# Kernel optimization log

Measured on AMD Instinct MI355X. Metric: run time of the kernel, lower is better.

Reference implementation:

```python
import jax, jax.numpy as jnp
import numpy as np

DIM = 768
NUM_HEADS = 12
HEAD_DIM = DIM // NUM_HEADS
SCALE = HEAD_DIM ** -0.5


def setup_inputs() -> dict:
    key = jax.random.key(0)
    ks = jax.random.split(key, 7)
    B, N = 4, 2048
    s = DIM ** -0.5
    return {
        "x": jax.random.normal(ks[0], (B, N, DIM), dtype=jnp.float32),
        "attn_bias": jax.random.normal(ks[1], (1, NUM_HEADS, N, N), dtype=jnp.float32),
        "Wq": jax.random.normal(ks[2], (DIM, DIM), dtype=jnp.float32) * s,
        "Wk": jax.random.normal(ks[3], (DIM, DIM), dtype=jnp.float32) * s,
        "Wv": jax.random.normal(ks[4], (DIM, DIM), dtype=jnp.float32) * s,
        "Wp": jax.random.normal(ks[5], (DIM, DIM), dtype=jnp.float32) * s,
        "bp": jax.random.normal(ks[6], (DIM,), dtype=jnp.float32) * 0.02,
    }


def reference(x, attn_bias, Wq, Wk, Wv, Wp, bp):
    B, N, C = x.shape
    # Linear layers use y = x @ W.T (torch convention); split heads: [B,H,N,D]
    def heads(y):
        return y.reshape(B, N, NUM_HEADS, HEAD_DIM).transpose(0, 2, 1, 3)
    q = heads(x @ Wq.T)
    k = heads(x @ Wk.T)
    v = heads(x @ Wv.T)
    attn = jnp.einsum("bhnd,bhmd->bhnm", q, k) * SCALE + attn_bias
    attn = jax.nn.softmax(attn, axis=-1)
    out = jnp.einsum("bhnm,bhmd->bhnd", attn, v)
    out = out.transpose(0, 2, 1, 3).reshape(B, N, C)
    return out @ Wp.T + bp
```

## Files before the change

kernel.cpp:

```cpp
#include <hip/hip_runtime.h>
#include <hip/hip_bf16.h>

#define NTOK 2048
#define NHEADS 12
#define HDIM 64
#define DIM 768
#define BATCH 4
#define SC2_    0.18033688011112042f
#define LOG2E_  1.4426950408889634f
#define SHIFT2_ 23.083120654223415f

typedef __attribute__((ext_vector_type(8))) short short8;
typedef __attribute__((ext_vector_type(4))) float f32x4;
typedef __attribute__((ext_vector_type(16))) float f32x16;

__device__ __forceinline__ short f2bf(float f) {
  union { float f; unsigned u; } v; v.f = f;
  unsigned r = v.u + 0x7fffu + ((v.u >> 16) & 1u);
  return (short)(r >> 16);
}

__device__ __forceinline__ f32x4 mfma_bf16(short8 a, short8 b, f32x4 c) {
  return __builtin_amdgcn_mfma_f32_16x16x32_bf16(a, b, c, 0, 0, 0);
}

__device__ __forceinline__ f32x16 mfma32(short8 a, short8 b, f32x16 c) {
  return __builtin_amdgcn_mfma_f32_32x32x16_bf16(a, b, c, 0, 0, 0);
}

__device__ __forceinline__ void gload_lds16(const void* g, void* l) {
  __builtin_amdgcn_global_load_lds((const __attribute__((address_space(1))) void*)g,
                                   (__attribute__((address_space(3))) void*)l, 16, 0, 0);
}

__device__ __forceinline__ float exp2_hw(float x) {
  float r; asm("v_exp_f32 %0, %1" : "=v"(r) : "v"(x)); return r;
}

__device__ __forceinline__ unsigned cvt_pk_bf16(float lo, float hi) {
  unsigned r; asm("v_cvt_pk_bf16_f32 %0, %1, %2" : "=v"(r) : "v"(lo), "v"(hi)); return r;
}

__global__ void cvt_x(const float* __restrict__ src, short* __restrict__ dst) {
  int i = blockIdx.x * 256 + threadIdx.x;
  float4 v = ((const float4*)src)[i];
  short4 o; o.x = f2bf(v.x); o.y = f2bf(v.y); o.z = f2bf(v.z); o.w = f2bf(v.w);
  ((short4*)dst)[i] = o;
}

__global__ void cvt_w(const float* __restrict__ w0, const float* __restrict__ w1,
                      const float* __restrict__ w2, const float* __restrict__ w3,
                      short* __restrict__ d0, short* __restrict__ d1,
                      short* __restrict__ d2, short* __restrict__ d3) {
  int i = blockIdx.x * 256 + threadIdx.x;
  const float* s = blockIdx.y == 0 ? w0 : blockIdx.y == 1 ? w1 : blockIdx.y == 2 ? w2 : w3;
  short* d = blockIdx.y == 0 ? d0 : blockIdx.y == 1 ? d1 : blockIdx.y == 2 ? d2 : d3;
  float4 v = ((const float4*)s)[i];
  short4 o; o.x = f2bf(v.x); o.y = f2bf(v.y); o.z = f2bf(v.z); o.w = f2bf(v.w);
  ((short4*)d)[i] = o;
}

__device__ __forceinline__ void gemm_mainloop(const short* __restrict__ A,
                                              const short* __restrict__ B,
                                              int mbase, int nbase,
                                              short* As, short* Bs,
                                              f32x4 (&acc)[4][4], int lane, int w) {
  int lr = lane & 15, lg = lane >> 4;
  int wr = w >> 1, wc = w & 1;
  for (int kb = 0; kb < DIM; kb += 64) {
    if (kb) __syncthreads();
#pragma unroll
    for (int c = 0; c < 4; ++c) {
      int row = w * 32 + c * 8 + (lane >> 3);
      int sch = (lane & 7) ^ (row & 7);
      gload_lds16(A + (size_t)(mbase + row) * DIM + kb + sch * 8, (char*)As + w * 4096 + c * 1024);
      gload_lds16(B + (size_t)(nbase + row) * DIM + kb + sch * 8, (char*)Bs + w * 4096 + c * 1024);
    }
    __syncthreads();
#pragma unroll
    for (int ks = 0; ks < 2; ++ks) {
      short8 af[4], bf[4];
#pragma unroll
      for (int i = 0; i < 4; ++i) {
        int row = wr * 64 + i * 16 + lr;
        int ch = (ks * 4 + lg) ^ (row & 7);
        af[i] = *(const short8*)(As + row * 64 + ch * 8);
      }
#pragma unroll
      for (int j = 0; j < 4; ++j) {
        int row = wc * 64 + j * 16 + lr;
        int ch = (ks * 4 + lg) ^ (row & 7);
        bf[j] = *(const short8*)(Bs + row * 64 + ch * 8);
      }
#pragma unroll
      for (int i = 0; i < 4; ++i)
#pragma unroll
        for (int j = 0; j < 4; ++j)
          acc[i][j] = mfma_bf16(af[i], bf[j], acc[i][j]);
    }
  }
}

__global__ __launch_bounds__(256, 2) void gemm_qkv(const short* __restrict__ xb,
    const short* __restrict__ wq, const short* __restrict__ wk, const short* __restrict__ wv,
    short* __restrict__ Qh, short* __restrict__ Kh, short* __restrict__ Vt) {
  __shared__ __align__(16) short As[128 * 64];
  __shared__ __align__(16) short Bs[128 * 64];
  int nt = blockIdx.x, mt = blockIdx.y, z = blockIdx.z;
  const short* B = z == 0 ? wq : (z == 1 ? wk : wv);
  int tid = threadIdx.x, lane = tid & 63, w = tid >> 6;
  f32x4 acc[4][4] = {};
  gemm_mainloop(xb, B, mt * 128, nt * 128, As, Bs, acc, lane, w);
  int lr = lane & 15, lg = lane >> 4, wr = w >> 1, wc = w & 1;
  if (z < 2) {
    short* dst = z == 0 ? Qh : Kh;
#pragma unroll
    for (int i = 0; i < 4; ++i)
#pragma unroll
      for (int j = 0; j < 4; ++j) {
        int m = mt * 128 + wr * 64 + i * 16 + lg * 4;
        int n = nt * 128 + wc * 64 + j * 16 + lr;
        int bb = m >> 11, nn = m & 2047, hh = n >> 6, d = n & 63;
        size_t base = (((size_t)bb * NHEADS + hh) * NTOK + nn) * HDIM + d;
#pragma unroll
        for (int r = 0; r < 4; ++r)
          dst[base + (size_t)r * HDIM] = f2bf(acc[i][j][r]);
      }
  } else {
#pragma unroll
    for (int i = 0; i < 4; ++i)
#pragma unroll
      for (int j = 0; j < 4; ++j) {
        int m = mt * 128 + wr * 64 + i * 16 + lg * 4;
        int n = nt * 128 + wc * 64 + j * 16 + lr;
        int bb = m >> 11, nn = m & 2047, hh = n >> 6, d = n & 63;
        short4 pk;
        pk.x = f2bf(acc[i][j][0]); pk.y = f2bf(acc[i][j][1]);
        pk.z = f2bf(acc[i][j][2]); pk.w = f2bf(acc[i][j][3]);
        *(short4*)(Vt + (((size_t)bb * NHEADS + hh) * HDIM + d) * NTOK + nn) = pk;
      }
  }
}


#define ATTN_BODY(T, CUR)                                                     \
  {                                                                           \
    const int kv = (T) * 64;                                                  \
    f32x4 bv[8];                                                              \
    _Pragma("unroll")                                                         \
    for (int g = 0; g < 8; ++g)                                               \
      bv[g] = *(const f32x4*)(Bb + kv + g * 8 + hi * 4);                      \
    if ((T) < NTOK / 64 - 1) {                                                \
      _Pragma("unroll")                                                       \
      for (int c = 0; c < 2; ++c) {                                           \
        int srow = (lane >> 3) ^ (w * 2 + c);                                 \
        int sch = (lane & 7) ^ srow;                                          \
        int row = w * 16 + c * 8 + (lane >> 3);                               \
        gload_lds16(K + (size_t)(kv + 64 + row) * HDIM + sch * 8,             \
                    (char*)Ks[(CUR) ^ 1] + w * 2048 + c * 1024);              \
        gload_lds16(V + (size_t)row * NTOK + kv + 64 + sch * 8,               \
                    (char*)Vs[(CUR) ^ 1] + w * 2048 + c * 1024);              \
      }                                                                       \
    }                                                                         \
    f32x16 sacc0 = {}, sacc1 = {};                                            \
    __builtin_amdgcn_s_setprio(1);                                            \
    _Pragma("unroll")                                                         \
    for (int i = 0; i < 4; ++i) {                                             \
      int srow0 = (ql & 7) ^ (ql >> 3);                                       \
      int srow1 = (ql & 7) ^ (4 + (ql >> 3));                                 \
      short8 kf0 = *(const short8*)(Ks[CUR] + ql * 64 + (((i * 2 + hi) ^ srow0) * 8)); \
      short8 kf1 = *(const short8*)(Ks[CUR] + (32 + ql) * 64 + (((i * 2 + hi) ^ srow1) * 8)); \
      sacc0 = mfma32(kf0, qf[i], sacc0);                                      \
      sacc1 = mfma32(kf1, qf[i], sacc1);                                      \
    }                                                                         \
    __builtin_amdgcn_s_setprio(0);                                            \
    _Pragma("unroll")                                                         \
    for (int kb = 0; kb < 2; ++kb) {                                          \
      float p[16];                                                            \
      _Pragma("unroll")                                                       \
      for (int rg = 0; rg < 16; ++rg) {                                       \
        float tb = fmaf(bv[kb * 4 + (rg >> 2)][rg & 3], LOG2E_, -SHIFT2_);    \
        p[rg] = exp2_hw(fmaf((kb ? sacc1[rg] : sacc0[rg]), SC2_, tb));        \
      }                                                                       \
      float ts = 0.f;                                                         \
      _Pragma("unroll")                                                       \
      for (int g = 0; g < 4; ++g)                                             \
        ts += (p[g * 4] + p[g * 4 + 1]) + (p[g * 4 + 2] + p[g * 4 + 3]);      \
      psum += ts;                                                             \
      unsigned Wd[4][2];                                                      \
      _Pragma("unroll")                                                       \
      for (int g = 0; g < 4; ++g) {                                           \
        Wd[g][0] = cvt_pk_bf16(p[g * 4], p[g * 4 + 1]);                       \
        Wd[g][1] = cvt_pk_bf16(p[g * 4 + 2], p[g * 4 + 3]);                   \
      }                                                                       \
      _Pragma("unroll")                                                       \
      for (int cc = 0; cc < 2; ++cc) {                                        \
        auto r0 = __builtin_amdgcn_permlane32_swap(Wd[cc * 2][0], Wd[cc * 2 + 1][0], false, false); \
        auto r1 = __builtin_amdgcn_permlane32_swap(Wd[cc * 2][1], Wd[cc * 2 + 1][1], false, false); \
        union { unsigned u[4]; short8 s; } pb;                                \
        pb.u[0] = r0[0]; pb.u[1] = r1[0]; pb.u[2] = r0[1]; pb.u[3] = r1[1];   \
        __builtin_amdgcn_s_setprio(1);                                        \
        {                                                                     \
          int srow0 = (ql & 7) ^ (ql >> 3);                                   \
          int srow1 = (ql & 7) ^ (4 + (ql >> 3));                             \
          short8 vf0 = *(const short8*)(Vs[CUR] + ql * 64 + (((kb * 4 + cc * 2 + hi) ^ srow0) * 8)); \
          short8 vf1 = *(const short8*)(Vs[CUR] + (32 + ql) * 64 + (((kb * 4 + cc * 2 + hi) ^ srow1) * 8)); \
          oacc0 = mfma32(vf0, pb.s, oacc0);                                   \
          oacc1 = mfma32(vf1, pb.s, oacc1);                                   \
        }                                                                     \
        __builtin_amdgcn_s_setprio(0);                                        \
      }                                                                       \
    }                                                                         \
    __syncthreads();                                                          \
  }

__global__ __launch_bounds__(256, 3) void attn_fused(const short* __restrict__ Qh,
    const short* __restrict__ Kh, const short* __restrict__ Vt,
    const float* __restrict__ bias, short* __restrict__ Ob) {
  __shared__ __align__(16) short Ks[2][64 * 64];
  __shared__ __align__(16) short Vs[2][64 * 64];
  int d0 = blockIdx.x;
  int wg = (d0 & 7) * 96 + (d0 >> 3);
  int b = wg & 3, qb = (wg >> 2) & 15, h = wg >> 6;
  int tid = threadIdx.x, lane = tid & 63, w = tid >> 6;
  int ql = lane & 31, hi = lane >> 5;

  const short* Q = Qh + ((size_t)b * NHEADS + h) * NTOK * HDIM;
  const short* K = Kh + ((size_t)b * NHEADS + h) * NTOK * HDIM;
  const short* V = Vt + ((size_t)b * NHEADS + h) * HDIM * NTOK;
  int qrow = qb * 128 + w * 32 + ql;
  const float* Bb = bias + ((size_t)h * NTOK + qrow) * NTOK;

  short8 qf[4];
#pragma unroll
  for (int i = 0; i < 4; ++i)
    qf[i] = *(const short8*)(Q + (size_t)qrow * HDIM + i * 16 + hi * 8);

  float psum = 0.f;
  f32x16 oacc0 = {}, oacc1 = {};

#pragma unroll
  for (int c = 0; c < 2; ++c) {
    int srow = (lane >> 3) ^ (w * 2 + c);
    int sch = (lane & 7) ^ srow;
    int row = w * 16 + c * 8 + (lane >> 3);
    gload_lds16(K + (size_t)row * HDIM + sch * 8, (char*)Ks[0] + w * 2048 + c * 1024);
    gload_lds16(V + (size_t)row * NTOK + sch * 8, (char*)Vs[0] + w * 2048 + c * 1024);
  }
  __syncthreads();

  for (int t = 0; t < NTOK / 64; t += 2) {
    ATTN_BODY(t, 0)
    ATTN_BODY(t + 1, 1)
  }

  float fs = psum + __shfl_xor(psum, 32);
  float inv = 1.f / fs;
  size_t obase = ((size_t)b * NTOK + qrow) * DIM + h * HDIM;
#pragma unroll
  for (int g = 0; g < 4; ++g) {
    unsigned u0 = cvt_pk_bf16(oacc0[g * 4] * inv, oacc0[g * 4 + 1] * inv);
    unsigned u1 = cvt_pk_bf16(oacc0[g * 4 + 2] * inv, oacc0[g * 4 + 3] * inv);
    uint2 pk0; pk0.x = u0; pk0.y = u1;
    *(uint2*)(Ob + obase + g * 8 + hi * 4) = pk0;
    unsigned u2 = cvt_pk_bf16(oacc1[g * 4] * inv, oacc1[g * 4 + 1] * inv);
    unsigned u3 = cvt_pk_bf16(oacc1[g * 4 + 2] * inv, oacc1[g * 4 + 3] * inv);
    uint2 pk1; pk1.x = u2; pk1.y = u3;
    *(uint2*)(Ob + obase + 32 + g * 8 + hi * 4) = pk1;
  }
}

__global__ __launch_bounds__(256, 2) void gemm_proj(const short* __restrict__ Ob,
    const short* __restrict__ wp, const float* __restrict__ bp, float* __restrict__ out) {
  __shared__ __align__(16) short As[128 * 64];
  __shared__ __align__(16) short Bs[128 * 64];
  int nt = blockIdx.x, mt = blockIdx.y;
  int tid = threadIdx.x, lane = tid & 63, w = tid >> 6;
  f32x4 acc[4][4] = {};
  gemm_mainloop(Ob, wp, mt * 128, nt * 128, As, Bs, acc, lane, w);
  int lr = lane & 15, lg = lane >> 4, wr = w >> 1, wc = w & 1;
#pragma unroll
  for (int j = 0; j < 4; ++j) {
    int n = nt * 128 + wc * 64 + j * 16 + lr;
    float bpv = bp[n];
#pragma unroll
    for (int i = 0; i < 4; ++i) {
      int m = mt * 128 + wr * 64 + i * 16 + lg * 4;
#pragma unroll
      for (int r = 0; r < 4; ++r)
        out[(size_t)(m + r) * DIM + n] = acc[i][j][r] + bpv;
    }
  }
}

extern "C" void kernel_launch(void* const* d_in, const int* in_sizes, int n_in,
                              void* d_out, int out_size, void* d_ws, size_t ws_size,
                              hipStream_t stream) {
  const float* x    = (const float*)d_in[0];
  const float* bias = (const float*)d_in[1];
  const float* Wq   = (const float*)d_in[2];
  const float* Wk   = (const float*)d_in[3];
  const float* Wv   = (const float*)d_in[4];
  const float* Wp   = (const float*)d_in[5];
  const float* bp   = (const float*)d_in[6];
  float* out = (float*)d_out;

  char* ws = (char*)d_ws;
  short* xb  = (short*)(ws);
  short* wqb = (short*)(ws + 12582912);
  short* wkb = (short*)(ws + 13762560);
  short* wvb = (short*)(ws + 14942208);
  short* wpb = (short*)(ws + 16121856);
  short* Qh  = (short*)(ws + 17301504);
  short* Kh  = (short*)(ws + 29884416);
  short* Vt  = (short*)(ws + 42467328);
  short* Ob  = (short*)(ws + 55050240);

  cvt_x<<<6144, 256, 0, stream>>>(x, xb);
  cvt_w<<<dim3(576, 4), 256, 0, stream>>>(Wq, Wk, Wv, Wp, wqb, wkb, wvb, wpb);
  gemm_qkv<<<dim3(6, 64, 3), 256, 0, stream>>>(xb, wqb, wkb, wvb, Qh, Kh, Vt);
  attn_fused<<<768, 256, 0, stream>>>(Qh, Kh, Vt, bias, Ob);
  gemm_proj<<<dim3(6, 64), 256, 0, stream>>>(Ob, wpb, bp, out);
}
```

Baseline: 214.4 us.

## Stage attention bias through LDS, fold Q scale into GEMM, MFMA row sums

Reworks the fused attention loop to use 32-key tiles and prefetches the fp32 bias tile into LDS with async global-to-LDS loads, double-buffered alongside K and V with XOR swizzles. Previously each thread loaded bias straight from global memory. The softmax scale is folded into Q at the QKV GEMM epilogue, which removes one FMA per score. The fixed max-shift constant is dropped, so exp2 runs unshifted and risks overflow if scores are large. Row sums now come from an extra MFMA against a vector of ones instead of scalar adds and a final shuffle, and the smaller tiles mean more barriers per key.

```diff
diff --git a/kernel.cpp b/kernel.cpp
--- a/kernel.cpp
+++ b/kernel.cpp
@@ -8,7 +8,6 @@
 #define BATCH 4
 #define SC2_    0.18033688011112042f
 #define LOG2E_  1.4426950408889634f
-#define SHIFT2_ 23.083120654223415f
 
 typedef __attribute__((ext_vector_type(8))) short short8;
 typedef __attribute__((ext_vector_type(4))) float f32x4;
@@ -40,6 +39,8 @@
 __device__ __forceinline__ unsigned cvt_pk_bf16(float lo, float hi) {
   unsigned r; asm("v_cvt_pk_bf16_f32 %0, %1, %2" : "=v"(r) : "v"(lo), "v"(hi)); return r;
 }
+
+__device__ __forceinline__ int swz(int r) { return (r ^ (r >> 3)) & 7; }
 
 __global__ void cvt_x(const float* __restrict__ src, short* __restrict__ dst) {
   int i = blockIdx.x * 256 + threadIdx.x;
@@ -114,6 +115,7 @@
   int lr = lane & 15, lg = lane >> 4, wr = w >> 1, wc = w & 1;
   if (z < 2) {
     short* dst = z == 0 ? Qh : Kh;
+    float sc = z == 0 ? SC2_ : 1.f;
 #pragma unroll
     for (int i = 0; i < 4; ++i)
 #pragma unroll
@@ -124,7 +126,7 @@
         size_t base = (((size_t)bb * NHEADS + hh) * NTOK + nn) * HDIM + d;
 #pragma unroll
         for (int r = 0; r < 4; ++r)
-          dst[base + (size_t)r * HDIM] = f2bf(acc[i][j][r]);
+          dst[base + (size_t)r * HDIM] = f2bf(acc[i][j][r] * sc);
       }
   } else {
 #pragma unroll
@@ -142,83 +144,12 @@
   }
 }
 
-
-#define ATTN_BODY(T, CUR)                                                     \
-  {                                                                           \
-    const int kv = (T) * 64;                                                  \
-    f32x4 bv[8];                                                              \
-    _Pragma("unroll")                                                         \
-    for (int g = 0; g < 8; ++g)                                               \
-      bv[g] = *(const f32x4*)(Bb + kv + g * 8 + hi * 4);                      \
-    if ((T) < NTOK / 64 - 1) {                                                \
-      _Pragma("unroll")                                                       \
-      for (int c = 0; c < 2; ++c) {                                           \
-        int srow = (lane >> 3) ^ (w * 2 + c);                                 \
-        int sch = (lane & 7) ^ srow;                                          \
-        int row = w * 16 + c * 8 + (lane >> 3);                               \
-        gload_lds16(K + (size_t)(kv + 64 + row) * HDIM + sch * 8,             \
-                    (char*)Ks[(CUR) ^ 1] + w * 2048 + c * 1024);              \
-        gload_lds16(V + (size_t)row * NTOK + kv + 64 + sch * 8,               \
-                    (char*)Vs[(CUR) ^ 1] + w * 2048 + c * 1024);              \
-      }                                                                       \
-    }                                                                         \
-    f32x16 sacc0 = {}, sacc1 = {};                                            \
-    __builtin_amdgcn_s_setprio(1);                                            \
-    _Pragma("unroll")                                                         \
-    for (int i = 0; i < 4; ++i) {                                             \
-      int srow0 = (ql & 7) ^ (ql >> 3);                                       \
-      int srow1 = (ql & 7) ^ (4 + (ql >> 3));                                 \
-      short8 kf0 = *(const short8*)(Ks[CUR] + ql * 64 + (((i * 2 + hi) ^ srow0) * 8)); \
-      short8 kf1 = *(const short8*)(Ks[CUR] + (32 + ql) * 64 + (((i * 2 + hi) ^ srow1) * 8)); \
-      sacc0 = mfma32(kf0, qf[i], sacc0);                                      \
-      sacc1 = mfma32(kf1, qf[i], sacc1);                                      \
-    }                                                                         \
-    __builtin_amdgcn_s_setprio(0);                                            \
-    _Pragma("unroll")                                                         \
-    for (int kb = 0; kb < 2; ++kb) {                                          \
-      float p[16];                                                            \
-      _Pragma("unroll")                                                       \
-      for (int rg = 0; rg < 16; ++rg) {                                       \
-        float tb = fmaf(bv[kb * 4 + (rg >> 2)][rg & 3], LOG2E_, -SHIFT2_);    \
-        p[rg] = exp2_hw(fmaf((kb ? sacc1[rg] : sacc0[rg]), SC2_, tb));        \
-      }                                                                       \
-      float ts = 0.f;                                                         \
-      _Pragma("unroll")                                                       \
-      for (int g = 0; g < 4; ++g)                                             \
-        ts += (p[g * 4] + p[g * 4 + 1]) + (p[g * 4 + 2] + p[g * 4 + 3]);      \
-      psum += ts;                                                             \
-      unsigned Wd[4][2];                                                      \
-      _Pragma("unroll")                                                       \
-      for (int g = 0; g < 4; ++g) {                                           \
-        Wd[g][0] = cvt_pk_bf16(p[g * 4], p[g * 4 + 1]);                       \
-        Wd[g][1] = cvt_pk_bf16(p[g * 4 + 2], p[g * 4 + 3]);                   \
-      }                                                                       \
-      _Pragma("unroll")                                                       \
-      for (int cc = 0; cc < 2; ++cc) {                                        \
-        auto r0 = __builtin_amdgcn_permlane32_swap(Wd[cc * 2][0], Wd[cc * 2 + 1][0], false, false); \
-        auto r1 = __builtin_amdgcn_permlane32_swap(Wd[cc * 2][1], Wd[cc * 2 + 1][1], false, false); \
-        union { unsigned u[4]; short8 s; } pb;                                \
-        pb.u[0] = r0[0]; pb.u[1] = r1[0]; pb.u[2] = r0[1]; pb.u[3] = r1[1];   \
-        __builtin_amdgcn_s_setprio(1);                                        \
-        {                                                                     \
-          int srow0 = (ql & 7) ^ (ql >> 3);                                   \
-          int srow1 = (ql & 7) ^ (4 + (ql >> 3));                             \
-          short8 vf0 = *(const short8*)(Vs[CUR] + ql * 64 + (((kb * 4 + cc * 2 + hi) ^ srow0) * 8)); \
-          short8 vf1 = *(const short8*)(Vs[CUR] + (32 + ql) * 64 + (((kb * 4 + cc * 2 + hi) ^ srow1) * 8)); \
-          oacc0 = mfma32(vf0, pb.s, oacc0);                                   \
-          oacc1 = mfma32(vf1, pb.s, oacc1);                                   \
-        }                                                                     \
-        __builtin_amdgcn_s_setprio(0);                                        \
-      }                                                                       \
-    }                                                                         \
-    __syncthreads();                                                          \
-  }
-
 __global__ __launch_bounds__(256, 3) void attn_fused(const short* __restrict__ Qh,
     const short* __restrict__ Kh, const short* __restrict__ Vt,
     const float* __restrict__ bias, short* __restrict__ Ob) {
-  __shared__ __align__(16) short Ks[2][64 * 64];
-  __shared__ __align__(16) short Vs[2][64 * 64];
+  __shared__ __align__(16) short Ks[2][32 * 64];
+  __shared__ __align__(16) short Vs[2][32 * 64];
+  __shared__ __align__(16) float Bsh[2][128 * 32];
   int d0 = blockIdx.x;
   int wg = (d0 & 7) * 96 + (d0 >> 3);
   int b = wg & 3, qb = (wg >> 2) & 15, h = wg >> 6;
@@ -229,33 +160,125 @@
   const short* K = Kh + ((size_t)b * NHEADS + h) * NTOK * HDIM;
   const short* V = Vt + ((size_t)b * NHEADS + h) * HDIM * NTOK;
   int qrow = qb * 128 + w * 32 + ql;
-  const float* Bb = bias + ((size_t)h * NTOK + qrow) * NTOK;
+  const float* Bg = bias + ((size_t)h * NTOK + qb * 128) * NTOK;
 
   short8 qf[4];
 #pragma unroll
   for (int i = 0; i < 4; ++i)
     qf[i] = *(const short8*)(Q + (size_t)qrow * HDIM + i * 16 + hi * 8);
 
-  float psum = 0.f;
-  f32x16 oacc0 = {}, oacc1 = {};
-
-#pragma unroll
-  for (int c = 0; c < 2; ++c) {
-    int srow = (lane >> 3) ^ (w * 2 + c);
-    int sch = (lane & 7) ^ srow;
-    int row = w * 16 + c * 8 + (lane >> 3);
-    gload_lds16(K + (size_t)row * HDIM + sch * 8, (char*)Ks[0] + w * 2048 + c * 1024);
-    gload_lds16(V + (size_t)row * NTOK + sch * 8, (char*)Vs[0] + w * 2048 + c * 1024);
-  }
+  short8 onesv;
+#pragma unroll
+  for (int i = 0; i < 8; ++i) onesv[i] = (short)0x3F80;
+
+  f32x16 oacc0 = {}, oacc1 = {}, sumacc = {};
+
+  int l8 = lane >> 3, s7 = lane & 7;
+
+  int krow = w * 8 + l8;
+  const short* Ksrc = K + (size_t)krow * HDIM + (s7 ^ swz(krow)) * 8;
+  int vrp = w * 8 + l8;
+  int vu = s7 ^ swz(vrp);
+  const short* Vsrc = V + (size_t)(vrp * 2 + (vu >> 2)) * NTOK + (vu & 3) * 8;
+  int br0 = w * 32 + 0 + l8, br1 = w * 32 + 8 + l8, br2 = w * 32 + 16 + l8, br3 = w * 32 + 24 + l8;
+  const float* Bsrc0 = Bg + (size_t)br0 * NTOK + (s7 ^ swz(br0)) * 4;
+  const float* Bsrc1 = Bg + (size_t)br1 * NTOK + (s7 ^ swz(br1)) * 4;
+  const float* Bsrc2 = Bg + (size_t)br2 * NTOK + (s7 ^ swz(br2)) * 4;
+  const float* Bsrc3 = Bg + (size_t)br3 * NTOK + (s7 ^ swz(br3)) * 4;
+  char* Kdst = (char*)Ks[0] + w * 1024;
+  char* Vdst = (char*)Vs[0] + w * 1024;
+  char* Bdst = (char*)Bsh[0] + w * 4096;
+
+  int sq = swz(ql);
+  const short* ka0 = Ks[0] + ql * 64 + ((0 + hi) ^ sq) * 8;
+  const short* ka1 = Ks[0] + ql * 64 + ((2 + hi) ^ sq) * 8;
+  const short* ka2 = Ks[0] + ql * 64 + ((4 + hi) ^ sq) * 8;
+  const short* ka3 = Ks[0] + ql * 64 + ((6 + hi) ^ sq) * 8;
+  int brow = w * 32 + ql, sb = swz(brow);
+  const float* ba0 = Bsh[0] + brow * 32 + ((0 + hi) ^ sb) * 4;
+  const float* ba1 = Bsh[0] + brow * 32 + ((2 + hi) ^ sb) * 4;
+  const float* ba2 = Bsh[0] + brow * 32 + ((4 + hi) ^ sb) * 4;
+  const float* ba3 = Bsh[0] + brow * 32 + ((6 + hi) ^ sb) * 4;
+  int rp0 = ql >> 1, rp1 = 16 + (ql >> 1);
+  int sv0 = swz(rp0), sv1 = swz(rp1);
+  int q4 = (ql & 1) * 4 + hi;
+  const short* va00 = Vs[0] + rp0 * 64 + ((q4 + 0) ^ sv0) * 8;
+  const short* va01 = Vs[0] + rp1 * 64 + ((q4 + 0) ^ sv1) * 8;
+  const short* va10 = Vs[0] + rp0 * 64 + ((q4 + 2) ^ sv0) * 8;
+  const short* va11 = Vs[0] + rp1 * 64 + ((q4 + 2) ^ sv1) * 8;
+
+#define STAGE(CUR)                                                            \
+  {                                                                           \
+    gload_lds16(Ksrc, Kdst + (CUR) * 4096);  Ksrc += 32 * HDIM;               \
+    gload_lds16(Vsrc, Vdst + (CUR) * 4096);  Vsrc += 32;                      \
+    gload_lds16(Bsrc0, Bdst + (CUR) * 16384);           Bsrc0 += 32;          \
+    gload_lds16(Bsrc1, Bdst + (CUR) * 16384 + 1024);    Bsrc1 += 32;          \
+    gload_lds16(Bsrc2, Bdst + (CUR) * 16384 + 2048);    Bsrc2 += 32;          \
+    gload_lds16(Bsrc3, Bdst + (CUR) * 16384 + 3072);    Bsrc3 += 32;          \
+  }
+
+#define BODY(T, CUR)                                                          \
+  {                                                                           \
+    if ((T) < NTOK / 32 - 1) STAGE((CUR) ^ 1)                                 \
+    short8 kf0 = *(const short8*)(ka0 + (CUR) * 2048);                        \
+    short8 kf1 = *(const short8*)(ka1 + (CUR) * 2048);                        \
+    short8 kf2 = *(const short8*)(ka2 + (CUR) * 2048);                        \
+    short8 kf3 = *(const short8*)(ka3 + (CUR) * 2048);                        \
+    f32x4 bv0 = *(const f32x4*)(ba0 + (CUR) * 4096);                          \
+    f32x4 bv1 = *(const f32x4*)(ba1 + (CUR) * 4096);                          \
+    f32x4 bv2 = *(const f32x4*)(ba2 + (CUR) * 4096);                          \
+    f32x4 bv3 = *(const f32x4*)(ba3 + (CUR) * 4096);                          \
+    short8 vA = *(const short8*)(va00 + (CUR) * 2048);                        \
+    short8 vB = *(const short8*)(va01 + (CUR) * 2048);                        \
+    short8 vC = *(const short8*)(va10 + (CUR) * 2048);                        \
+    short8 vD = *(const short8*)(va11 + (CUR) * 2048);                        \
+    f32x16 sacc = {};                                                         \
+    __builtin_amdgcn_s_setprio(1);                                            \
+    sacc = mfma32(kf0, qf[0], sacc);                                          \
+    sacc = mfma32(kf1, qf[1], sacc);                                          \
+    sacc = mfma32(kf2, qf[2], sacc);                                          \
+    sacc = mfma32(kf3, qf[3], sacc);                                          \
+    __builtin_amdgcn_s_setprio(0);                                            \
+    float p[16];                                                              \
+    _Pragma("unroll")                                                         \
+    for (int r = 0; r < 4; ++r) {                                             \
+      p[0 + r]  = exp2_hw(fmaf(bv0[r], LOG2E_, sacc[0 + r]));                 \
+      p[4 + r]  = exp2_hw(fmaf(bv1[r], LOG2E_, sacc[4 + r]));                 \
+      p[8 + r]  = exp2_hw(fmaf(bv2[r], LOG2E_, sacc[8 + r]));                 \
+      p[12 + r] = exp2_hw(fmaf(bv3[r], LOG2E_, sacc[12 + r]));                \
+    }                                                                         \
+    unsigned Wd[4][2];                                                        \
+    _Pragma("unroll")                                                         \
+    for (int g = 0; g < 4; ++g) {                                             \
+      Wd[g][0] = cvt_pk_bf16(p[g * 4], p[g * 4 + 1]);                         \
+      Wd[g][1] = cvt_pk_bf16(p[g * 4 + 2], p[g * 4 + 3]);                     \
+    }                                                                         \
+    _Pragma("unroll")                                                         \
+    for (int cc = 0; cc < 2; ++cc) {                                          \
+      auto r0 = __builtin_amdgcn_permlane32_swap(Wd[cc * 2][0], Wd[cc * 2 + 1][0], false, false); \
+      auto r1 = __builtin_amdgcn_permlane32_swap(Wd[cc * 2][1], Wd[cc * 2 + 1][1], false, false); \
+      union { unsigned u[4]; short8 s; } pb;                                  \
+      pb.u[0] = r0[0]; pb.u[1] = r1[0]; pb.u[2] = r0[1]; pb.u[3] = r1[1];     \
+      __builtin_amdgcn_s_setprio(1);                                          \
+      oacc0 = mfma32(cc ? vC : vA, pb.s, oacc0);                              \
+      oacc1 = mfma32(cc ? vD : vB, pb.s, oacc1);                              \
+      sumacc = mfma32(onesv, pb.s, sumacc);                                   \
+      __builtin_amdgcn_s_setprio(0);                                          \
+    }                                                                         \
+    __syncthreads();                                                          \
+  }
+
+  STAGE(0)
   __syncthreads();
 
-  for (int t = 0; t < NTOK / 64; t += 2) {
-    ATTN_BODY(t, 0)
-    ATTN_BODY(t + 1, 1)
-  }
-
-  float fs = psum + __shfl_xor(psum, 32);
-  float inv = 1.f / fs;
+  for (int t = 0; t < NTOK / 32; t += 2) {
+    BODY(t, 0)
+    BODY(t + 1, 1)
+  }
+#undef BODY
+#undef STAGE
+
+  float inv = 1.f / sumacc[0];
   size_t obase = ((size_t)b * NTOK + qrow) * DIM + h * HDIM;
 #pragma unroll
   for (int g = 0; g < 4; ++g) {
```

New measurement: 196.1 us, median of 2. -8.5%, faster.
